# Optimization experiments

Hardware: AMD Instinct MI355X
Metric: run time of the kernel (lower is better)

Reference implementation:

```python
import jax, jax.numpy as jnp
import numpy as np
import math

DIM = 2048
NH = 16
Q_RANK = 1536
KV_RANK = 512
D_NOPE = 128
D_ROPE = 64
D_V = 128
EPS = 1e-6
B, S = 2, 2048
THETA = 10000.0


def _rms_norm(x, w):
    return x * jax.lax.rsqrt(jnp.mean(x * x, axis=-1, keepdims=True) + EPS) * w


def _rope_cos_sin(seq_len, d):
    inv_freq = 1.0 / (THETA ** (jnp.arange(0, d, 2, dtype=jnp.float32) / d))
    t = jnp.arange(seq_len, dtype=jnp.float32)
    freqs = jnp.outer(t, inv_freq)  # (s, d/2)
    return jnp.cos(freqs), jnp.sin(freqs)


def _apply_rope(x, cos, sin):
    # x: (b, s, h, d), rotate interleaved pairs (llama-style complex rotation)
    x1 = x[..., 0::2]
    x2 = x[..., 1::2]
    c = cos[None, :, None, :]
    s = sin[None, :, None, :]
    o1 = x1 * c - x2 * s
    o2 = x1 * s + x2 * c
    return jnp.stack([o1, o2], axis=-1).reshape(x.shape)


def setup_inputs() -> dict:
    key = jax.random.key(0)
    ks = jax.random.split(key, 10)
    sd = 0.02
    return {
        "x": jax.random.normal(ks[0], (B, S, DIM), dtype=jnp.float32),
        # torch nn.Linear weights: (out_features, in_features), y = x @ W.T
        "wq_down": jax.random.normal(ks[1], (Q_RANK, DIM), dtype=jnp.float32) * sd,
        "wq_up": jax.random.normal(ks[2], (NH * D_NOPE, Q_RANK), dtype=jnp.float32) * sd,
        "wq_rope": jax.random.normal(ks[3], (NH * D_ROPE, Q_RANK), dtype=jnp.float32) * sd,
        "q_norm_w": jnp.ones((Q_RANK,), dtype=jnp.float32),
        "wkv_down": jax.random.normal(ks[4], (KV_RANK, DIM), dtype=jnp.float32) * sd,
        "kv_norm_w": jnp.ones((KV_RANK,), dtype=jnp.float32),
        "wkv_up": jax.random.normal(ks[5], (NH * (D_NOPE + D_V), KV_RANK), dtype=jnp.float32) * sd,
        "wk_rope": jax.random.normal(ks[6], (D_ROPE, DIM), dtype=jnp.float32) * sd,
        "wo": jax.random.normal(ks[7], (DIM, NH * D_V), dtype=jnp.float32) * sd,
    }


def reference(x, wq_down, wq_up, wq_rope, q_norm_w, wkv_down, kv_norm_w, wkv_up, wk_rope, wo):
    bs, seq_len, _ = x.shape
    # --- Q low-rank path ---
    q_c = _rms_norm(x @ wq_down.T, q_norm_w)                    # (b, s, q_rank)
    q_nope = (q_c @ wq_up.T).reshape(bs, seq_len, NH, D_NOPE)
    q_pe = (q_c @ wq_rope.T).reshape(bs, seq_len, NH, D_ROPE)
    # --- KV low-rank path ---
    kv_c = _rms_norm(x @ wkv_down.T, kv_norm_w)                 # (b, s, kv_rank)
    kv_up = (kv_c @ wkv_up.T).reshape(bs, seq_len, NH, D_NOPE + D_V)
    k_nope = kv_up[..., :D_NOPE]
    v = kv_up[..., D_NOPE:]                                     # (b, s, h, dv)
    # shared single-head rope key
    k_rope_shared = (x @ wk_rope.T).reshape(bs, seq_len, 1, D_ROPE)
    # --- partial-dim RoPE ---
    cos, sin = _rope_cos_sin(seq_len, D_ROPE)
    q_pe = _apply_rope(q_pe, cos, sin)
    k_rope_shared = _apply_rope(k_rope_shared, cos, sin)
    k_rope = jnp.broadcast_to(k_rope_shared, (bs, seq_len, NH, D_ROPE))
    # --- concat nope + rope dims ---
    q = jnp.concatenate([q_nope, q_pe], axis=-1)                # (b, s, h, dn+dr)
    k = jnp.concatenate([k_nope, k_rope], axis=-1)
    scale = 1.0 / math.sqrt(D_NOPE + D_ROPE)
    scores = jnp.einsum("bqhd,bkhd->bhqk", q, k) * scale        # (b, h, s, s)
    causal = jnp.tril(jnp.ones((seq_len, seq_len), dtype=bool))
    scores = jnp.where(causal[None, None], scores, -jnp.inf)
    probs = jax.nn.softmax(scores.astype(jnp.float32), axis=-1).astype(q.dtype)
    out = jnp.einsum("bhqk,bkhd->bqhd", probs, v)               # (b, s, h, dv)
    out = out.reshape(bs, seq_len, NH * D_V)
    return out @ wo.T


if __name__ == "__main__":
    inp = setup_inputs()
    y = jax.jit(reference)(**inp)
    print(y.shape, y.dtype)
```

## Files before the change

### kernel.cpp

```cpp
#include <hip/hip_runtime.h>
#include <hip/hip_bf16.h>
#include <math.h>

#define NHH 16
#define SS  2048
#define TT  4096
#define DQK 192
#define QSCALE 0.07216878364870322f
#define ROPE_C 0.28782313662425574f

typedef __bf16 bf16x8 __attribute__((ext_vector_type(8)));
typedef float f32x4 __attribute__((ext_vector_type(4)));

#define GLOAD16(gp, lp) __builtin_amdgcn_global_load_lds( \
    (const __attribute__((address_space(1))) void*)(gp),  \
    (__attribute__((address_space(3))) void*)(lp), 16, 0, 0)

#define SEG0 8388608
#define SEG1 11534336
#define SEG2 12582912
#define SEG3 12713984
#define SEG4 15859712
#define SEG5 17432576
#define SEG6 19529728
#define SEG7 23724032

__global__ __launch_bounds__(256) void cast_all(
        const float* __restrict__ x, const float* __restrict__ wqd,
        const float* __restrict__ wkvd, const float* __restrict__ wkr,
        const float* __restrict__ wqu, const float* __restrict__ wqr,
        const float* __restrict__ wkvu, const float* __restrict__ wo,
        __bf16* __restrict__ xb, __bf16* __restrict__ wqd_b,
        __bf16* __restrict__ wkvd_b, __bf16* __restrict__ wkr_b,
        __bf16* __restrict__ wqu_b, __bf16* __restrict__ wqr_b,
        __bf16* __restrict__ wkvu_b, __bf16* __restrict__ wo_b) {
    const int i = (blockIdx.x * 256 + threadIdx.x) * 8;
    const float* src;
    __bf16* dst;
    int off;
    if (i < SEG0)      { src = x;    dst = xb;     off = i; }
    else if (i < SEG1) { src = wqd;  dst = wqd_b;  off = i - SEG0; }
    else if (i < SEG2) { src = wkvd; dst = wkvd_b; off = i - SEG1; }
    else if (i < SEG3) { src = wkr;  dst = wkr_b;  off = i - SEG2; }
    else if (i < SEG4) { src = wqu;  dst = wqu_b;  off = i - SEG3; }
    else if (i < SEG5) { src = wqr;  dst = wqr_b;  off = i - SEG4; }
    else if (i < SEG6) { src = wkvu; dst = wkvu_b; off = i - SEG5; }
    else               { src = wo;   dst = wo_b;   off = i - SEG6; }
    const float4 a = *(const float4*)(src + off);
    const float4 b = *(const float4*)(src + off + 4);
    __bf16 o[8] = {(__bf16)a.x, (__bf16)a.y, (__bf16)a.z, (__bf16)a.w,
                   (__bf16)b.x, (__bf16)b.y, (__bf16)b.z, (__bf16)b.w};
    *(bf16x8*)(dst + off) = *(const bf16x8*)o;
}

__global__ __launch_bounds__(256) void rmsnorm_k(const float* __restrict__ in,
                                                 __bf16* __restrict__ out,
                                                 const float* __restrict__ w, int N) {
    const int row = blockIdx.x;
    const float* xr = in + (size_t)row * N;
    float ss = 0.f;
    for (int i = threadIdx.x; i < N; i += 256) {
        float v = xr[i];
        ss += v * v;
    }
    __shared__ float red[256];
    red[threadIdx.x] = ss;
    __syncthreads();
    for (int s = 128; s > 0; s >>= 1) {
        if (threadIdx.x < s) red[threadIdx.x] += red[threadIdx.x + s];
        __syncthreads();
    }
    const float scale = rsqrtf(red[0] / (float)N + 1e-6f);
    __bf16* orow = out + (size_t)row * N;
    for (int i = threadIdx.x; i < N; i += 256) orow[i] = (__bf16)(xr[i] * scale * w[i]);
}

template<int MODE>
__global__ __launch_bounds__(512, 1) void gemm8(
        const __bf16* __restrict__ A,
        const __bf16* __restrict__ W0, const __bf16* __restrict__ W1,
        const __bf16* __restrict__ W2,
        float* __restrict__ F0, float* __restrict__ F1,
        __bf16* __restrict__ B0, __bf16* __restrict__ B1,
        int M, int N, int K) {
    __shared__ __bf16 lds[3 * 24576];
    const int tid = threadIdx.x;
    const int w = tid >> 6, l = tid & 63;
    const int lr = l & 15, lg = l >> 4;
    const int wm = w >> 2, wn = w & 3;
    const int m0 = blockIdx.y * 128;
    const int n0 = blockIdx.x * 256;

    const int srow = (w << 3) + (l >> 3);
    const int scol = (l & 7) << 3;
    const int sswz = ((srow >> 1) & 7) << 3;
    const int csw  = scol ^ sswz;

    const __bf16* aptr[2];
#pragma unroll
    for (int a = 0; a < 2; ++a)
        aptr[a] = A + (size_t)(m0 + a * 64 + srow) * K + csw;

    const __bf16* bptr[4];
#pragma unroll
    for (int bb = 0; bb < 4; ++bb) {
        const int n = n0 + bb * 64 + srow;
        const __bf16* wp;
        if (MODE == 0) {
            if (n < 1536)      wp = W0 + (size_t)n * K;
            else if (n < 2048) wp = W1 + (size_t)(n - 1536) * K;
            else if (n < 2112) wp = W2 + (size_t)(n - 2048) * K;
            else               wp = W0;
        } else if (MODE == 1) {
            wp = (n < 2048) ? W0 + (size_t)n * K : W1 + (size_t)(n - 2048) * K;
        } else {
            wp = W0 + (size_t)n * K;
        }
        bptr[bb] = wp + csw;
    }

    auto stA = [&](int t2, int a) {
        GLOAD16(aptr[a] + (size_t)t2 * 64,
                &lds[(t2 % 3) * 24576 + a * 4096 + tid * 8]);
    };
    auto stB = [&](int t2, int b) {
        GLOAD16(bptr[b] + (size_t)t2 * 64,
                &lds[(t2 % 3) * 24576 + 8192 + b * 4096 + tid * 8]);
    };

    const int rswz = ((lr >> 1) & 7) << 3;

    f32x4 acc[4][4];
#pragma unroll
    for (int i = 0; i < 4; ++i)
#pragma unroll
        for (int j = 0; j < 4; ++j) acc[i][j] = (f32x4){0.f, 0.f, 0.f, 0.f};

    const int NT = K >> 6;
#pragma unroll
    for (int t = 0; t < 2; ++t) {
        stA(t, 0); stA(t, 1);
        stB(t, 0); stB(t, 1); stB(t, 2); stB(t, 3);
    }

    for (int t = 0; t < NT; ++t) {
        if (t + 1 < NT) asm volatile("s_waitcnt vmcnt(6)" ::: "memory");
        else            asm volatile("s_waitcnt vmcnt(0)" ::: "memory");
        __builtin_amdgcn_s_barrier();

        const __bf16* As_ = &lds[(t % 3) * 24576];
        const __bf16* Bs_ = As_ + 8192;
        const bool st = (t + 2 < NT);
        const int t2 = t + 2;

        bf16x8 fa[2][2], fb0[2][2], fb1[2][2];

#pragma unroll
        for (int i = 0; i < 2; ++i)
#pragma unroll
            for (int kk = 0; kk < 2; ++kk)
                fa[i][kk] = *(const bf16x8*)&As_[(wm * 64 + i * 16 + lr) * 64 +
                                                 ((kk * 32 + lg * 8) ^ rswz)];
#pragma unroll
        for (int j = 0; j < 2; ++j)
#pragma unroll
            for (int kk = 0; kk < 2; ++kk)
                fb0[j][kk] = *(const bf16x8*)&Bs_[(wn * 64 + j * 16 + lr) * 64 +
                                                  ((kk * 32 + lg * 8) ^ rswz)];
        if (st) { stA(t2, 0); stA(t2, 1); }
        __builtin_amdgcn_s_barrier();
        __builtin_amdgcn_s_setprio(1);
#pragma unroll
        for (int i = 0; i < 2; ++i)
#pragma unroll
            for (int j = 0; j < 2; ++j)
#pragma unroll
                for (int kk = 0; kk < 2; ++kk)
                    acc[i][j] = __builtin_amdgcn_mfma_f32_16x16x32_bf16(fa[i][kk], fb0[j][kk], acc[i][j], 0, 0, 0);
        __builtin_amdgcn_s_setprio(0);
        __builtin_amdgcn_s_barrier();

#pragma unroll
        for (int j = 0; j < 2; ++j)
#pragma unroll
            for (int kk = 0; kk < 2; ++kk)
                fb1[j][kk] = *(const bf16x8*)&Bs_[(wn * 64 + (j + 2) * 16 + lr) * 64 +
                                                  ((kk * 32 + lg * 8) ^ rswz)];
        if (st) { stB(t2, 0); stB(t2, 1); }
        __builtin_amdgcn_s_barrier();
        __builtin_amdgcn_s_setprio(1);
#pragma unroll
        for (int i = 0; i < 2; ++i)
#pragma unroll
            for (int j = 0; j < 2; ++j)
#pragma unroll
                for (int kk = 0; kk < 2; ++kk)
                    acc[i][j + 2] = __builtin_amdgcn_mfma_f32_16x16x32_bf16(fa[i][kk], fb1[j][kk], acc[i][j + 2], 0, 0, 0);
        __builtin_amdgcn_s_setprio(0);
        __builtin_amdgcn_s_barrier();

#pragma unroll
        for (int i = 0; i < 2; ++i)
#pragma unroll
            for (int kk = 0; kk < 2; ++kk)
                fa[i][kk] = *(const bf16x8*)&As_[(wm * 64 + (i + 2) * 16 + lr) * 64 +
                                                 ((kk * 32 + lg * 8) ^ rswz)];
        if (st) { stB(t2, 2); stB(t2, 3); }
        __builtin_amdgcn_s_barrier();
        __builtin_amdgcn_s_setprio(1);
#pragma unroll
        for (int i = 0; i < 2; ++i)
#pragma unroll
            for (int j = 0; j < 2; ++j)
#pragma unroll
                for (int kk = 0; kk < 2; ++kk)
                    acc[i + 2][j + 2] = __builtin_amdgcn_mfma_f32_16x16x32_bf16(fa[i][kk], fb1[j][kk], acc[i + 2][j + 2], 0, 0, 0);
        __builtin_amdgcn_s_setprio(0);
        __builtin_amdgcn_s_barrier();

        __builtin_amdgcn_s_setprio(1);
#pragma unroll
        for (int i = 0; i < 2; ++i)
#pragma unroll
            for (int j = 0; j < 2; ++j)
#pragma unroll
                for (int kk = 0; kk < 2; ++kk)
                    acc[i + 2][j] = __builtin_amdgcn_mfma_f32_16x16x32_bf16(fa[i][kk], fb0[j][kk], acc[i + 2][j], 0, 0, 0);
        __builtin_amdgcn_s_setprio(0);
    }

#pragma unroll
    for (int i = 0; i < 4; ++i) {
#pragma unroll
        for (int j = 0; j < 4; ++j) {
#pragma unroll
            for (int r = 0; r < 4; ++r) {
                const int m = m0 + wm * 64 + i * 16 + lg * 4 + r;
                const int n = n0 + wn * 64 + j * 16 + lr;
                const float v = acc[i][j][r];
                float vp = 0.f;
                if (MODE == 0 || MODE == 1) vp = __shfl_xor(v, 1);
                if (MODE == 0) {
                    if (n < 1536) {
                        F0[(size_t)m * 1536 + n] = v;
                    } else if (n < 2048) {
                        F1[(size_t)m * 512 + (n - 1536)] = v;
                    } else if (n < 2112) {
                        const int jj = n - 2048;
                        const int fi = jj >> 1;
                        const int spos = m & (SS - 1);
                        const float freq = __expf(-ROPE_C * (float)fi);
                        const float ang = (float)spos * freq;
                        const float sn = __sinf(ang), cs = __cosf(ang);
                        const float o = (jj & 1) ? (vp * sn + v * cs) : (v * cs - vp * sn);
                        B0[(size_t)m * 64 + jj] = (__bf16)o;
                    }
                } else if (MODE == 1) {
                    if (n < 2048) {
                        B0[(size_t)m * 3072 + (n >> 7) * 192 + (n & 127)] = (__bf16)(v * QSCALE);
                    } else {
                        const int jj = n - 2048;
                        const int h = jj >> 6, dd = jj & 63;
                        const int fi = dd >> 1;
                        const int spos = m & (SS - 1);
                        const float freq = __expf(-ROPE_C * (float)fi);
                        const float ang = (float)spos * freq;
                        const float sn = __sinf(ang), cs = __cosf(ang);
                        const float o = (dd & 1) ? (vp * sn + v * cs) : (v * cs - vp * sn);
                        B0[(size_t)m * 3072 + h * 192 + 128 + dd] = (__bf16)(o * QSCALE);
                    }
                } else if (MODE == 2) {
                    const int h = n >> 8, off = n & 255;
                    if (off < 128)
                        B0[(size_t)m * 2048 + h * 128 + off] = (__bf16)v;
                    else
                        B1[(((size_t)(m >> 11) * NHH + h) * 128 + (off - 128)) * SS + (m & (SS - 1))] = (__bf16)v;
                } else {
                    F0[(size_t)m * N + n] = v;
                }
            }
        }
    }
}

__global__ __launch_bounds__(512, 1) void attn_mfma3(
        const __bf16* __restrict__ q, const __bf16* __restrict__ knope,
        const __bf16* __restrict__ krope, const __bf16* __restrict__ vT,
        __bf16* __restrict__ att) {
    const int flat = blockIdx.x;
    const int xcd = flat & 7;
    const int rest = flat >> 3;
    const int bx = rest & 7;
    const int g8 = xcd + 8 * (rest >> 3);
    const int h = g8 & 15;
    const int b = g8 >> 4;

    const int tid = threadIdx.x;
    const int w  = tid >> 6;
    const int l  = tid & 63;
    const int lr = l & 15;
    const int lg = l >> 4;

    __shared__ __bf16 Ks[2][64][200];
    __shared__ __bf16 Vs[2][128][72];
    __shared__ __bf16 Ps[8][16][72];

    const int tiles[2] = {bx, 15 - bx};

    bf16x8 sreg[5];
    auto stage_load = [&](int kv0) {
#pragma unroll
        for (int i = 0; i < 5; ++i) {
            const int gc = tid + 512 * i;
            if (gc < 1536) {
                const int row = gc / 24, cc = gc - row * 24;
                const size_t t = (size_t)(b * SS + kv0 + row);
                const __bf16* src = (cc < 16)
                    ? knope + t * 2048 + h * 128 + cc * 8
                    : krope + t * 64 + (cc - 16) * 8;
                sreg[i] = *(const bf16x8*)src;
            } else {
                const int c = gc - 1536;
                const int row = c >> 3, cc = c & 7;
                sreg[i] = *(const bf16x8*)(vT + (((size_t)b * NHH + h) * 128 + row) * SS
                                              + kv0 + cc * 8);
            }
        }
    };
    auto stage_write = [&](int bi) {
#pragma unroll
        for (int i = 0; i < 5; ++i) {
            const int gc = tid + 512 * i;
            if (gc < 1536) {
                const int row = gc / 24, cc = gc - row * 24;
                *(bf16x8*)&Ks[bi][row][cc * 8] = sreg[i];
            } else {
                const int c = gc - 1536;
                *(bf16x8*)&Vs[bi][c >> 3][(c & 7) * 8] = sreg[i];
            }
        }
    };

    stage_load(0);
    stage_write(0);
    __syncthreads();
    int cur = 0;

#pragma unroll
    for (int p = 0; p < 2; ++p) {
        const int rg0 = tiles[p] * 128 + w * 16;
        const int nkt = 2 * tiles[p] + 2;

        bf16x8 qf[6];
        {
            const __bf16* qb = q + (((size_t)(b * SS + rg0 + lr)) * NHH + h) * DQK + lg * 8;
#pragma unroll
            for (int c = 0; c < 6; ++c) qf[c] = *(const bf16x8*)(qb + c * 32);
        }

        f32x4 O[8];
#pragma unroll
        for (int n = 0; n < 8; ++n) O[n] = (f32x4){0.f, 0.f, 0.f, 0.f};
        float m_r[4], l_r[4];
#pragma unroll
        for (int r = 0; r < 4; ++r) { m_r[r] = -INFINITY; l_r[r] = 0.f; }

        for (int kt = 0; kt < nkt; ++kt) {
            const int kv0 = kt * 64;
            const bool hasNext = (kt + 1 < nkt) || (p == 0);
            const int nxt = (kt + 1 < nkt) ? (kt + 1) * 64 : 0;
            if (hasNext) stage_load(nxt);

            if (kv0 <= rg0 + 15) {
                f32x4 sc[4];
#pragma unroll
                for (int s = 0; s < 4; ++s) {
                    if (kv0 + s * 16 <= rg0 + 15) {
                        bf16x8 kf[6];
#pragma unroll
                        for (int c = 0; c < 6; ++c)
                            kf[c] = *(const bf16x8*)&Ks[cur][s * 16 + lr][c * 32 + lg * 8];
                        f32x4 a = (f32x4){0.f, 0.f, 0.f, 0.f};
                        __builtin_amdgcn_s_setprio(1);
#pragma unroll
                        for (int c = 0; c < 6; ++c)
                            a = __builtin_amdgcn_mfma_f32_16x16x32_bf16(qf[c], kf[c], a, 0, 0, 0);
                        __builtin_amdgcn_s_setprio(0);
                        sc[s] = a;
                    } else {
                        sc[s] = (f32x4){-INFINITY, -INFINITY, -INFINITY, -INFINITY};
                    }
                }
#pragma unroll
                for (int s = 0; s < 4; ++s) {
                    const int col = kv0 + s * 16 + lr;
#pragma unroll
                    for (int r = 0; r < 4; ++r)
                        if (col > rg0 + lg * 4 + r) sc[s][r] = -INFINITY;
                }
                float mt[4];
#pragma unroll
                for (int r = 0; r < 4; ++r) {
                    float m = fmaxf(fmaxf(sc[0][r], sc[1][r]), fmaxf(sc[2][r], sc[3][r]));
                    m = fmaxf(m, __shfl_xor(m, 1));
                    m = fmaxf(m, __shfl_xor(m, 2));
                    m = fmaxf(m, __shfl_xor(m, 4));
                    m = fmaxf(m, __shfl_xor(m, 8));
                    mt[r] = m;
                }
                const bool ok = (mt[0] <= m_r[0] + 8.f) && (mt[1] <= m_r[1] + 8.f) &&
                                (mt[2] <= m_r[2] + 8.f) && (mt[3] <= m_r[3] + 8.f);
                if (!__all(ok)) {
#pragma unroll
                    for (int r = 0; r < 4; ++r) {
                        const float mn = fmaxf(m_r[r], mt[r]);
                        const float al = __expf(m_r[r] - mn);
                        m_r[r] = mn;
                        l_r[r] *= al;
#pragma unroll
                        for (int n = 0; n < 8; ++n) O[n][r] *= al;
                    }
                }
#pragma unroll
                for (int s = 0; s < 4; ++s) {
#pragma unroll
                    for (int r = 0; r < 4; ++r) {
                        const float pv = __expf(sc[s][r] - m_r[r]);
                        sc[s][r] = pv;
                        Ps[w][lg * 4 + r][s * 16 + lr] = (__bf16)pv;
                    }
                }
#pragma unroll
                for (int r = 0; r < 4; ++r) {
                    float ls = (sc[0][r] + sc[1][r]) + (sc[2][r] + sc[3][r]);
                    ls += __shfl_xor(ls, 1);
                    ls += __shfl_xor(ls, 2);
                    ls += __shfl_xor(ls, 4);
                    ls += __shfl_xor(ls, 8);
                    l_r[r] += ls;
                }
                bf16x8 pf[2];
#pragma unroll
                for (int ks = 0; ks < 2; ++ks)
                    pf[ks] = *(const bf16x8*)&Ps[w][lr][ks * 32 + lg * 8];
#pragma unroll
                for (int n = 0; n < 8; ++n) {
                    bf16x8 v0 = *(const bf16x8*)&Vs[cur][n * 16 + lr][lg * 8];
                    bf16x8 v1 = *(const bf16x8*)&Vs[cur][n * 16 + lr][32 + lg * 8];
                    __builtin_amdgcn_s_setprio(1);
                    O[n] = __builtin_amdgcn_mfma_f32_16x16x32_bf16(pf[0], v0, O[n], 0, 0, 0);
                    O[n] = __builtin_amdgcn_mfma_f32_16x16x32_bf16(pf[1], v1, O[n], 0, 0, 0);
                    __builtin_amdgcn_s_setprio(0);
                }
            }

            if (hasNext) stage_write(cur ^ 1);
            __syncthreads();
            cur ^= 1;
        }

        float inv[4];
#pragma unroll
        for (int r = 0; r < 4; ++r) inv[r] = 1.0f / l_r[r];
#pragma unroll
        for (int n = 0; n < 8; ++n) {
#pragma unroll
            for (int r = 0; r < 4; ++r) {
                const size_t t = (size_t)(b * SS + rg0 + lg * 4 + r);
                att[(t * NHH + h) * 128 + n * 16 + lr] = (__bf16)(O[n][r] * inv[r]);
            }
        }
    }
}

extern "C" void kernel_launch(void* const* d_in, const int* in_sizes, int n_in,
                              void* d_out, int out_size, void* d_ws, size_t ws_size,
                              hipStream_t stream) {
    (void)in_sizes; (void)n_in; (void)out_size; (void)ws_size;
    const float* x        = (const float*)d_in[0];
    const float* wq_down  = (const float*)d_in[1];
    const float* wq_up    = (const float*)d_in[2];
    const float* wq_rope  = (const float*)d_in[3];
    const float* q_norm_w = (const float*)d_in[4];
    const float* wkv_down = (const float*)d_in[5];
    const float* kv_norm_w= (const float*)d_in[6];
    const float* wkv_up   = (const float*)d_in[7];
    const float* wk_rope  = (const float*)d_in[8];
    const float* wo       = (const float*)d_in[9];
    float* out = (float*)d_out;

    char* ws = (char*)d_ws;
    float*  q_c   = (float*)(ws + 0);
    __bf16* att   = (__bf16*)(ws + 0);
    float*  kv_c  = (float*)(ws + 25165824);
    __bf16* xb    = (__bf16*)(ws + 33554432);
    __bf16* vT    = (__bf16*)(ws + 33554432);
    __bf16* qc_b  = (__bf16*)(ws + 50331648);
    __bf16* kvc_b = (__bf16*)(ws + 62914560);
    __bf16* krope = (__bf16*)(ws + 67108864);
    __bf16* qbuf  = (__bf16*)(ws + 67633152);
    __bf16* wqd_b = (__bf16*)(ws + 92798976);
    __bf16* wqu_b = (__bf16*)(ws + 99090432);
    __bf16* wqr_b = (__bf16*)(ws + 105381888);
    __bf16* wkvd_b= (__bf16*)(ws + 108527616);
    __bf16* wkvu_b= (__bf16*)(ws + 110624768);
    __bf16* wkr_b = (__bf16*)(ws + 114819072);
    __bf16* wo_b  = (__bf16*)(ws + 115081216);
    __bf16* knope = (__bf16*)d_out;

    const dim3 blk(256);

    cast_all<<<dim3(SEG7 / 2048), blk, 0, stream>>>(
        x, wq_down, wkv_down, wk_rope, wq_up, wq_rope, wkv_up, wo,
        xb, wqd_b, wkvd_b, wkr_b, wqu_b, wqr_b, wkvu_b, wo_b);

    gemm8<0><<<dim3(9, 32), dim3(512), 0, stream>>>(xb, wqd_b, wkvd_b, wkr_b,
                                                    q_c, kv_c, krope, nullptr, TT, 2112, 2048);

    rmsnorm_k<<<dim3(TT), blk, 0, stream>>>(q_c, qc_b, q_norm_w, 1536);
    rmsnorm_k<<<dim3(TT), blk, 0, stream>>>(kv_c, kvc_b, kv_norm_w, 512);

    gemm8<1><<<dim3(12, 32), dim3(512), 0, stream>>>(qc_b, wqu_b, wqr_b, nullptr,
                                                     nullptr, nullptr, qbuf, nullptr, TT, 3072, 1536);

    gemm8<2><<<dim3(16, 32), dim3(512), 0, stream>>>(kvc_b, wkvu_b, nullptr, nullptr,
                                                     nullptr, nullptr, knope, vT, TT, 4096, 512);

    attn_mfma3<<<dim3(256), dim3(512), 0, stream>>>(qbuf, knope, krope, vT, att);

    gemm8<3><<<dim3(8, 32), dim3(512), 0, stream>>>(att, wo_b, nullptr, nullptr,
                                                    out, nullptr, nullptr, nullptr, TT, 2048, 2048);
}
```

Before: 370.6 us.

## Restructure attention blocks to 32 rows per wave and trim GEMM edge tiles

The attention kernel now gives each block one contiguous 256-row query tile, with each wave owning 32 rows (two 16-row groups), so every K/V tile loaded into shared memory serves twice as many queries. It replaces the earlier pairing of mirrored 128-row tiles used for causal balance, and the launch bound now allows two blocks per CU. Because each block's KV tile count grows with its query position, load is less balanced across blocks and register use is higher. The first GEMM uses a flat 1D grid in which the narrow 64-column rope tail blocks load only one B sub-tile and leave idle waves out of the MFMA work.

```diff
diff --git a/kernel.cpp b/kernel.cpp
--- a/kernel.cpp
+++ b/kernel.cpp
@@ -88,8 +88,18 @@
     const int w = tid >> 6, l = tid & 63;
     const int lr = l & 15, lg = l >> 4;
     const int wm = w >> 2, wn = w & 3;
-    const int m0 = blockIdx.y * 128;
-    const int n0 = blockIdx.x * 256;
+
+    int m0, n0, nlim;
+    if (MODE == 0) {
+        const int fb = blockIdx.x;
+        if (fb < 256) { m0 = (fb >> 3) * 128; n0 = (fb & 7) * 256; }
+        else          { m0 = (fb - 256) * 128; n0 = 2048; }
+        nlim = 2112 - n0;
+    } else {
+        m0 = blockIdx.y * 128; n0 = blockIdx.x * 256; nlim = 256;
+    }
+    const bool fullB = (nlim >= 256);
+    const bool wAct  = (wn * 64 < nlim);
 
     const int srow = (w << 3) + (l >> 3);
     const int scol = (l & 7) << 3;
@@ -140,12 +150,17 @@
 #pragma unroll
     for (int t = 0; t < 2; ++t) {
         stA(t, 0); stA(t, 1);
-        stB(t, 0); stB(t, 1); stB(t, 2); stB(t, 3);
+        stB(t, 0);
+        if (fullB) { stB(t, 1); stB(t, 2); stB(t, 3); }
     }
 
     for (int t = 0; t < NT; ++t) {
-        if (t + 1 < NT) asm volatile("s_waitcnt vmcnt(6)" ::: "memory");
-        else            asm volatile("s_waitcnt vmcnt(0)" ::: "memory");
+        if (t + 1 < NT) {
+            if (fullB) asm volatile("s_waitcnt vmcnt(6)" ::: "memory");
+            else       asm volatile("s_waitcnt vmcnt(3)" ::: "memory");
+        } else {
+            asm volatile("s_waitcnt vmcnt(0)" ::: "memory");
+        }
         __builtin_amdgcn_s_barrier();
 
         const __bf16* As_ = &lds[(t % 3) * 24576];
@@ -155,79 +170,95 @@
 
         bf16x8 fa[2][2], fb0[2][2], fb1[2][2];
 
-#pragma unroll
-        for (int i = 0; i < 2; ++i)
-#pragma unroll
-            for (int kk = 0; kk < 2; ++kk)
-                fa[i][kk] = *(const bf16x8*)&As_[(wm * 64 + i * 16 + lr) * 64 +
-                                                 ((kk * 32 + lg * 8) ^ rswz)];
-#pragma unroll
-        for (int j = 0; j < 2; ++j)
-#pragma unroll
-            for (int kk = 0; kk < 2; ++kk)
-                fb0[j][kk] = *(const bf16x8*)&Bs_[(wn * 64 + j * 16 + lr) * 64 +
-                                                  ((kk * 32 + lg * 8) ^ rswz)];
+        if (wAct) {
+#pragma unroll
+            for (int i = 0; i < 2; ++i)
+#pragma unroll
+                for (int kk = 0; kk < 2; ++kk)
+                    fa[i][kk] = *(const bf16x8*)&As_[(wm * 64 + i * 16 + lr) * 64 +
+                                                     ((kk * 32 + lg * 8) ^ rswz)];
+#pragma unroll
+            for (int j = 0; j < 2; ++j)
+#pragma unroll
+                for (int kk = 0; kk < 2; ++kk)
+                    fb0[j][kk] = *(const bf16x8*)&Bs_[(wn * 64 + j * 16 + lr) * 64 +
+                                                      ((kk * 32 + lg * 8) ^ rswz)];
+        }
         if (st) { stA(t2, 0); stA(t2, 1); }
         __builtin_amdgcn_s_barrier();
-        __builtin_amdgcn_s_setprio(1);
-#pragma unroll
-        for (int i = 0; i < 2; ++i)
+        if (wAct) {
+            __builtin_amdgcn_s_setprio(1);
+#pragma unroll
+            for (int i = 0; i < 2; ++i)
+#pragma unroll
+                for (int j = 0; j < 2; ++j)
+#pragma unroll
+                    for (int kk = 0; kk < 2; ++kk)
+                        acc[i][j] = __builtin_amdgcn_mfma_f32_16x16x32_bf16(fa[i][kk], fb0[j][kk], acc[i][j], 0, 0, 0);
+            __builtin_amdgcn_s_setprio(0);
+        }
+        __builtin_amdgcn_s_barrier();
+
+        if (wAct) {
 #pragma unroll
             for (int j = 0; j < 2; ++j)
 #pragma unroll
                 for (int kk = 0; kk < 2; ++kk)
-                    acc[i][j] = __builtin_amdgcn_mfma_f32_16x16x32_bf16(fa[i][kk], fb0[j][kk], acc[i][j], 0, 0, 0);
-        __builtin_amdgcn_s_setprio(0);
-        __builtin_amdgcn_s_barrier();
-
-#pragma unroll
-        for (int j = 0; j < 2; ++j)
-#pragma unroll
-            for (int kk = 0; kk < 2; ++kk)
-                fb1[j][kk] = *(const bf16x8*)&Bs_[(wn * 64 + (j + 2) * 16 + lr) * 64 +
-                                                  ((kk * 32 + lg * 8) ^ rswz)];
-        if (st) { stB(t2, 0); stB(t2, 1); }
-        __builtin_amdgcn_s_barrier();
-        __builtin_amdgcn_s_setprio(1);
-#pragma unroll
-        for (int i = 0; i < 2; ++i)
-#pragma unroll
-            for (int j = 0; j < 2; ++j)
+                    fb1[j][kk] = *(const bf16x8*)&Bs_[(wn * 64 + (j + 2) * 16 + lr) * 64 +
+                                                      ((kk * 32 + lg * 8) ^ rswz)];
+        }
+        if (st) { stB(t2, 0); if (fullB) stB(t2, 1); }
+        __builtin_amdgcn_s_barrier();
+        if (wAct) {
+            __builtin_amdgcn_s_setprio(1);
+#pragma unroll
+            for (int i = 0; i < 2; ++i)
+#pragma unroll
+                for (int j = 0; j < 2; ++j)
+#pragma unroll
+                    for (int kk = 0; kk < 2; ++kk)
+                        acc[i][j + 2] = __builtin_amdgcn_mfma_f32_16x16x32_bf16(fa[i][kk], fb1[j][kk], acc[i][j + 2], 0, 0, 0);
+            __builtin_amdgcn_s_setprio(0);
+        }
+        __builtin_amdgcn_s_barrier();
+
+        if (wAct) {
+#pragma unroll
+            for (int i = 0; i < 2; ++i)
 #pragma unroll
                 for (int kk = 0; kk < 2; ++kk)
-                    acc[i][j + 2] = __builtin_amdgcn_mfma_f32_16x16x32_bf16(fa[i][kk], fb1[j][kk], acc[i][j + 2], 0, 0, 0);
-        __builtin_amdgcn_s_setprio(0);
-        __builtin_amdgcn_s_barrier();
-
-#pragma unroll
-        for (int i = 0; i < 2; ++i)
-#pragma unroll
-            for (int kk = 0; kk < 2; ++kk)
-                fa[i][kk] = *(const bf16x8*)&As_[(wm * 64 + (i + 2) * 16 + lr) * 64 +
-                                                 ((kk * 32 + lg * 8) ^ rswz)];
-        if (st) { stB(t2, 2); stB(t2, 3); }
-        __builtin_amdgcn_s_barrier();
-        __builtin_amdgcn_s_setprio(1);
-#pragma unroll
-        for (int i = 0; i < 2; ++i)
-#pragma unroll
-            for (int j = 0; j < 2; ++j)
-#pragma unroll
-                for (int kk = 0; kk < 2; ++kk)
-                    acc[i + 2][j + 2] = __builtin_amdgcn_mfma_f32_16x16x32_bf16(fa[i][kk], fb1[j][kk], acc[i + 2][j + 2], 0, 0, 0);
-        __builtin_amdgcn_s_setprio(0);
-        __builtin_amdgcn_s_barrier();
-
-        __builtin_amdgcn_s_setprio(1);
-#pragma unroll
-        for (int i = 0; i < 2; ++i)
-#pragma unroll
-            for (int j = 0; j < 2; ++j)
-#pragma unroll
-                for (int kk = 0; kk < 2; ++kk)
-                    acc[i + 2][j] = __builtin_amdgcn_mfma_f32_16x16x32_bf16(fa[i][kk], fb0[j][kk], acc[i + 2][j], 0, 0, 0);
-        __builtin_amdgcn_s_setprio(0);
-    }
+                    fa[i][kk] = *(const bf16x8*)&As_[(wm * 64 + (i + 2) * 16 + lr) * 64 +
+                                                     ((kk * 32 + lg * 8) ^ rswz)];
+        }
+        if (st && fullB) { stB(t2, 2); stB(t2, 3); }
+        __builtin_amdgcn_s_barrier();
+        if (wAct) {
+            __builtin_amdgcn_s_setprio(1);
+#pragma unroll
+            for (int i = 0; i < 2; ++i)
+#pragma unroll
+                for (int j = 0; j < 2; ++j)
+#pragma unroll
+                    for (int kk = 0; kk < 2; ++kk)
+                        acc[i + 2][j + 2] = __builtin_amdgcn_mfma_f32_16x16x32_bf16(fa[i][kk], fb1[j][kk], acc[i + 2][j + 2], 0, 0, 0);
+            __builtin_amdgcn_s_setprio(0);
+        }
+        __builtin_amdgcn_s_barrier();
+
+        if (wAct) {
+            __builtin_amdgcn_s_setprio(1);
+#pragma unroll
+            for (int i = 0; i < 2; ++i)
+#pragma unroll
+                for (int j = 0; j < 2; ++j)
+#pragma unroll
+                    for (int kk = 0; kk < 2; ++kk)
+                        acc[i + 2][j] = __builtin_amdgcn_mfma_f32_16x16x32_bf16(fa[i][kk], fb0[j][kk], acc[i + 2][j], 0, 0, 0);
+            __builtin_amdgcn_s_setprio(0);
+        }
+    }
+
+    if (!wAct) return;
 
 #pragma unroll
     for (int i = 0; i < 4; ++i) {
@@ -283,15 +314,15 @@
     }
 }
 
-__global__ __launch_bounds__(512, 1) void attn_mfma3(
+__global__ __launch_bounds__(512, 2) void attn_mfma4(
         const __bf16* __restrict__ q, const __bf16* __restrict__ knope,
         const __bf16* __restrict__ krope, const __bf16* __restrict__ vT,
         __bf16* __restrict__ att) {
     const int flat = blockIdx.x;
     const int xcd = flat & 7;
-    const int rest = flat >> 3;
-    const int bx = rest & 7;
-    const int g8 = xcd + 8 * (rest >> 3);
+    const int a0 = flat >> 3;
+    const int t = a0 & 7;
+    const int g8 = ((a0 >> 3) << 3) | xcd;
     const int h = g8 & 15;
     const int b = g8 >> 4;
 
@@ -303,9 +334,10 @@
 
     __shared__ __bf16 Ks[2][64][200];
     __shared__ __bf16 Vs[2][128][72];
-    __shared__ __bf16 Ps[8][16][72];
-
-    const int tiles[2] = {bx, 15 - bx};
+    __shared__ __bf16 Ps[8][2][16][72];
+
+    const int rg0 = t * 256 + w * 32;
+    const int nkt = 4 * t + 4;
 
     bf16x8 sreg[5];
     auto stage_load = [&](int kv0) {
@@ -314,10 +346,10 @@
             const int gc = tid + 512 * i;
             if (gc < 1536) {
                 const int row = gc / 24, cc = gc - row * 24;
-                const size_t t = (size_t)(b * SS + kv0 + row);
+                const size_t tt = (size_t)(b * SS + kv0 + row);
                 const __bf16* src = (cc < 16)
-                    ? knope + t * 2048 + h * 128 + cc * 8
-                    : krope + t * 64 + (cc - 16) * 8;
+                    ? knope + tt * 2048 + h * 128 + cc * 8
+                    : krope + tt * 64 + (cc - 16) * 8;
                 sreg[i] = *(const bf16x8*)src;
             } else {
                 const int c = gc - 1536;
@@ -341,133 +373,159 @@
         }
     };
 
+    bf16x8 qf[2][6];
+#pragma unroll
+    for (int grp = 0; grp < 2; ++grp) {
+        const __bf16* qb = q + (((size_t)(b * SS + rg0 + grp * 16 + lr)) * NHH + h) * DQK + lg * 8;
+#pragma unroll
+        for (int c = 0; c < 6; ++c) qf[grp][c] = *(const bf16x8*)(qb + c * 32);
+    }
+
+    f32x4 O[2][8];
+    float m_r[2][4], l_r[2][4];
+#pragma unroll
+    for (int grp = 0; grp < 2; ++grp) {
+#pragma unroll
+        for (int n = 0; n < 8; ++n) O[grp][n] = (f32x4){0.f, 0.f, 0.f, 0.f};
+#pragma unroll
+        for (int r = 0; r < 4; ++r) { m_r[grp][r] = -INFINITY; l_r[grp][r] = 0.f; }
+    }
+
     stage_load(0);
     stage_write(0);
     __syncthreads();
     int cur = 0;
 
-#pragma unroll
-    for (int p = 0; p < 2; ++p) {
-        const int rg0 = tiles[p] * 128 + w * 16;
-        const int nkt = 2 * tiles[p] + 2;
-
-        bf16x8 qf[6];
-        {
-            const __bf16* qb = q + (((size_t)(b * SS + rg0 + lr)) * NHH + h) * DQK + lg * 8;
-#pragma unroll
-            for (int c = 0; c < 6; ++c) qf[c] = *(const bf16x8*)(qb + c * 32);
-        }
-
-        f32x4 O[8];
-#pragma unroll
-        for (int n = 0; n < 8; ++n) O[n] = (f32x4){0.f, 0.f, 0.f, 0.f};
-        float m_r[4], l_r[4];
-#pragma unroll
-        for (int r = 0; r < 4; ++r) { m_r[r] = -INFINITY; l_r[r] = 0.f; }
-
-        for (int kt = 0; kt < nkt; ++kt) {
-            const int kv0 = kt * 64;
-            const bool hasNext = (kt + 1 < nkt) || (p == 0);
-            const int nxt = (kt + 1 < nkt) ? (kt + 1) * 64 : 0;
-            if (hasNext) stage_load(nxt);
-
-            if (kv0 <= rg0 + 15) {
-                f32x4 sc[4];
-#pragma unroll
-                for (int s = 0; s < 4; ++s) {
-                    if (kv0 + s * 16 <= rg0 + 15) {
-                        bf16x8 kf[6];
-#pragma unroll
-                        for (int c = 0; c < 6; ++c)
-                            kf[c] = *(const bf16x8*)&Ks[cur][s * 16 + lr][c * 32 + lg * 8];
-                        f32x4 a = (f32x4){0.f, 0.f, 0.f, 0.f};
-                        __builtin_amdgcn_s_setprio(1);
-#pragma unroll
-                        for (int c = 0; c < 6; ++c)
-                            a = __builtin_amdgcn_mfma_f32_16x16x32_bf16(qf[c], kf[c], a, 0, 0, 0);
-                        __builtin_amdgcn_s_setprio(0);
-                        sc[s] = a;
-                    } else {
-                        sc[s] = (f32x4){-INFINITY, -INFINITY, -INFINITY, -INFINITY};
+    for (int kt = 0; kt < nkt; ++kt) {
+        const int kv0 = kt * 64;
+        const bool hasNext = (kt + 1 < nkt);
+        if (hasNext) stage_load(kv0 + 64);
+
+        const bool ga0 = kv0 <= rg0 + 15;
+        const bool ga1 = kv0 <= rg0 + 31;
+        if (ga1) {
+            f32x4 sc[2][4];
+#pragma unroll
+            for (int s = 0; s < 4; ++s) {
+                const int colb = kv0 + s * 16;
+                if (colb <= rg0 + 31) {
+                    bf16x8 kf[6];
+#pragma unroll
+                    for (int c = 0; c < 6; ++c)
+                        kf[c] = *(const bf16x8*)&Ks[cur][s * 16 + lr][c * 32 + lg * 8];
+                    __builtin_amdgcn_s_setprio(1);
+#pragma unroll
+                    for (int grp = 0; grp < 2; ++grp) {
+                        if (colb <= rg0 + grp * 16 + 15) {
+                            f32x4 acc = (f32x4){0.f, 0.f, 0.f, 0.f};
+#pragma unroll
+                            for (int c = 0; c < 6; ++c)
+                                acc = __builtin_amdgcn_mfma_f32_16x16x32_bf16(qf[grp][c], kf[c], acc, 0, 0, 0);
+                            sc[grp][s] = acc;
+                        } else {
+                            sc[grp][s] = (f32x4){-INFINITY, -INFINITY, -INFINITY, -INFINITY};
+                        }
                     }
-                }
+                    __builtin_amdgcn_s_setprio(0);
+                } else {
+                    sc[0][s] = (f32x4){-INFINITY, -INFINITY, -INFINITY, -INFINITY};
+                    sc[1][s] = (f32x4){-INFINITY, -INFINITY, -INFINITY, -INFINITY};
+                }
+            }
+
+#pragma unroll
+            for (int grp = 0; grp < 2; ++grp) {
+                const bool ga = (grp == 0) ? ga0 : ga1;
+                if (!ga) continue;
+                const int rg = rg0 + grp * 16;
 #pragma unroll
                 for (int s = 0; s < 4; ++s) {
                     const int col = kv0 + s * 16 + lr;
 #pragma unroll
                     for (int r = 0; r < 4; ++r)
-                        if (col > rg0 + lg * 4 + r) sc[s][r] = -INFINITY;
+                        if (col > rg + lg * 4 + r) sc[grp][s][r] = -INFINITY;
                 }
                 float mt[4];
 #pragma unroll
                 for (int r = 0; r < 4; ++r) {
-                    float m = fmaxf(fmaxf(sc[0][r], sc[1][r]), fmaxf(sc[2][r], sc[3][r]));
+                    float m = fmaxf(fmaxf(sc[grp][0][r], sc[grp][1][r]),
+                                    fmaxf(sc[grp][2][r], sc[grp][3][r]));
                     m = fmaxf(m, __shfl_xor(m, 1));
                     m = fmaxf(m, __shfl_xor(m, 2));
                     m = fmaxf(m, __shfl_xor(m, 4));
                     m = fmaxf(m, __shfl_xor(m, 8));
                     mt[r] = m;
                 }
-                const bool ok = (mt[0] <= m_r[0] + 8.f) && (mt[1] <= m_r[1] + 8.f) &&
-                                (mt[2] <= m_r[2] + 8.f) && (mt[3] <= m_r[3] + 8.f);
+                const bool ok = (mt[0] <= m_r[grp][0] + 8.f) && (mt[1] <= m_r[grp][1] + 8.f) &&
+                                (mt[2] <= m_r[grp][2] + 8.f) && (mt[3] <= m_r[grp][3] + 8.f);
                 if (!__all(ok)) {
 #pragma unroll
                     for (int r = 0; r < 4; ++r) {
-                        const float mn = fmaxf(m_r[r], mt[r]);
-                        const float al = __expf(m_r[r] - mn);
-                        m_r[r] = mn;
-                        l_r[r] *= al;
-#pragma unroll
-                        for (int n = 0; n < 8; ++n) O[n][r] *= al;
+                        const float mn = fmaxf(m_r[grp][r], mt[r]);
+                        const float al = __expf(m_r[grp][r] - mn);
+                        m_r[grp][r] = mn;
+                        l_r[grp][r] *= al;
+#pragma unroll
+                        for (int n = 0; n < 8; ++n) O[grp][n][r] *= al;
                     }
                 }
 #pragma unroll
                 for (int s = 0; s < 4; ++s) {
 #pragma unroll
                     for (int r = 0; r < 4; ++r) {
-                        const float pv = __expf(sc[s][r] - m_r[r]);
-                        sc[s][r] = pv;
-                        Ps[w][lg * 4 + r][s * 16 + lr] = (__bf16)pv;
+                        const float pv = __expf(sc[grp][s][r] - m_r[grp][r]);
+                        sc[grp][s][r] = pv;
+                        Ps[w][grp][lg * 4 + r][s * 16 + lr] = (__bf16)pv;
                     }
                 }
 #pragma unroll
                 for (int r = 0; r < 4; ++r) {
-                    float ls = (sc[0][r] + sc[1][r]) + (sc[2][r] + sc[3][r]);
+                    float ls = (sc[grp][0][r] + sc[grp][1][r]) + (sc[grp][2][r] + sc[grp][3][r]);
                     ls += __shfl_xor(ls, 1);
                     ls += __shfl_xor(ls, 2);
                     ls += __shfl_xor(ls, 4);
                     ls += __shfl_xor(ls, 8);
-                    l_r[r] += ls;
-                }
-                bf16x8 pf[2];
+                    l_r[grp][r] += ls;
+                }
+            }
+
+            bf16x8 pf[2][2];
+#pragma unroll
+            for (int grp = 0; grp < 2; ++grp)
 #pragma unroll
                 for (int ks = 0; ks < 2; ++ks)
-                    pf[ks] = *(const bf16x8*)&Ps[w][lr][ks * 32 + lg * 8];
-#pragma unroll
-                for (int n = 0; n < 8; ++n) {
-                    bf16x8 v0 = *(const bf16x8*)&Vs[cur][n * 16 + lr][lg * 8];
-                    bf16x8 v1 = *(const bf16x8*)&Vs[cur][n * 16 + lr][32 + lg * 8];
-                    __builtin_amdgcn_s_setprio(1);
-                    O[n] = __builtin_amdgcn_mfma_f32_16x16x32_bf16(pf[0], v0, O[n], 0, 0, 0);
-                    O[n] = __builtin_amdgcn_mfma_f32_16x16x32_bf16(pf[1], v1, O[n], 0, 0, 0);
-                    __builtin_amdgcn_s_setprio(0);
-                }
-            }
-
-            if (hasNext) stage_write(cur ^ 1);
-            __syncthreads();
-            cur ^= 1;
-        }
-
+                    pf[grp][ks] = *(const bf16x8*)&Ps[w][grp][lr][ks * 32 + lg * 8];
+#pragma unroll
+            for (int n = 0; n < 8; ++n) {
+                bf16x8 v0 = *(const bf16x8*)&Vs[cur][n * 16 + lr][lg * 8];
+                bf16x8 v1 = *(const bf16x8*)&Vs[cur][n * 16 + lr][32 + lg * 8];
+                __builtin_amdgcn_s_setprio(1);
+                O[0][n] = __builtin_amdgcn_mfma_f32_16x16x32_bf16(pf[0][0], v0, O[0][n], 0, 0, 0);
+                O[0][n] = __builtin_amdgcn_mfma_f32_16x16x32_bf16(pf[0][1], v1, O[0][n], 0, 0, 0);
+                if (ga1) {
+                    O[1][n] = __builtin_amdgcn_mfma_f32_16x16x32_bf16(pf[1][0], v0, O[1][n], 0, 0, 0);
+                    O[1][n] = __builtin_amdgcn_mfma_f32_16x16x32_bf16(pf[1][1], v1, O[1][n], 0, 0, 0);
+                }
+                __builtin_amdgcn_s_setprio(0);
+            }
+        }
+
+        if (hasNext) stage_write(cur ^ 1);
+        __syncthreads();
+        cur ^= 1;
+    }
+
+#pragma unroll
+    for (int grp = 0; grp < 2; ++grp) {
         float inv[4];
 #pragma unroll
-        for (int r = 0; r < 4; ++r) inv[r] = 1.0f / l_r[r];
+        for (int r = 0; r < 4; ++r) inv[r] = 1.0f / l_r[grp][r];
 #pragma unroll
         for (int n = 0; n < 8; ++n) {
 #pragma unroll
             for (int r = 0; r < 4; ++r) {
-                const size_t t = (size_t)(b * SS + rg0 + lg * 4 + r);
-                att[(t * NHH + h) * 128 + n * 16 + lr] = (__bf16)(O[n][r] * inv[r]);
+                const size_t tt = (size_t)(b * SS + rg0 + grp * 16 + lg * 4 + r);
+                att[(tt * NHH + h) * 128 + n * 16 + lr] = (__bf16)(O[grp][n][r] * inv[r]);
             }
         }
     }
@@ -514,8 +572,8 @@
         x, wq_down, wkv_down, wk_rope, wq_up, wq_rope, wkv_up, wo,
         xb, wqd_b, wkvd_b, wkr_b, wqu_b, wqr_b, wkvu_b, wo_b);
 
-    gemm8<0><<<dim3(9, 32), dim3(512), 0, stream>>>(xb, wqd_b, wkvd_b, wkr_b,
-                                                    q_c, kv_c, krope, nullptr, TT, 2112, 2048);
+    gemm8<0><<<dim3(288), dim3(512), 0, stream>>>(xb, wqd_b, wkvd_b, wkr_b,
+                                                  q_c, kv_c, krope, nullptr, TT, 2112, 2048);
 
     rmsnorm_k<<<dim3(TT), blk, 0, stream>>>(q_c, qc_b, q_norm_w, 1536);
     rmsnorm_k<<<dim3(TT), blk, 0, stream>>>(kv_c, kvc_b, kv_norm_w, 512);
@@ -526,7 +584,7 @@
     gemm8<2><<<dim3(16, 32), dim3(512), 0, stream>>>(kvc_b, wkvu_b, nullptr, nullptr,
                                                      nullptr, nullptr, knope, vT, TT, 4096, 512);
 
-    attn_mfma3<<<dim3(256), dim3(512), 0, stream>>>(qbuf, knope, krope, vT, att);
+    attn_mfma4<<<dim3(256), dim3(512), 0, stream>>>(qbuf, knope, krope, vT, att);
 
     gemm8<3><<<dim3(8, 32), dim3(512), 0, stream>>>(att, wo_b, nullptr, nullptr,
                                                     out, nullptr, nullptr, nullptr, TT, 2048, 2048);
```

New measurement: 413.7 us. 11.6% more time.
